# Performance work log

Measured on AMD Instinct MI355X. Metric: run time of the kernel, lower is better.

The kernel has to match this reference:

```python
import jax, jax.numpy as jnp
import numpy as np

DECAY = 0.8
BETA = 0.25
EPS = 1e-05
CODEBOOK_SIZE = 16384
CODEBOOK_DIM = 256


def setup_inputs() -> dict:
    key = jax.random.key(0)
    k1, k2 = jax.random.split(key)
    z = jax.random.normal(k1, (16, 256, 32, 32), dtype=jnp.float32)
    # EmbeddingEMA init: weight = randn(K, D) / K; embed_avg = weight.clone(); cluster_size = 0
    weight = jax.random.normal(k2, (CODEBOOK_SIZE, CODEBOOK_DIM), dtype=jnp.float32) / CODEBOOK_SIZE
    cluster_size = jnp.zeros((CODEBOOK_SIZE,), dtype=jnp.float32)
    embed_avg = weight
    return {"z": z, "weight": weight, "cluster_size": cluster_size, "embed_avg": embed_avg}


def reference(z, weight, cluster_size, embed_avg):
    K, D = weight.shape
    # b c h w -> b h w c
    zt = jnp.transpose(z, (0, 2, 3, 1))
    zf = zt.reshape(-1, D)  # [N, D]

    # squared-distance matrix [N, K]: |z|^2 + |w|^2 - 2 z.wT
    d = (jnp.sum(zf * zf, axis=1, keepdims=True)
         + jnp.sum(weight * weight, axis=1)
         - 2.0 * jnp.einsum('nd,kd->nk', zf, weight))
    token = jnp.argmin(d, axis=1)  # [N]

    z_q = weight[token].reshape(zt.shape)  # embedding lookup

    # training-mode EMA updates (scatter-add of one-hot assignments)
    counts = jax.ops.segment_sum(jnp.ones_like(token, dtype=zf.dtype), token, num_segments=K)
    embed_sum = jax.ops.segment_sum(zf, token, num_segments=K)  # one_hot.T @ zf
    cluster_new = DECAY * cluster_size + (1.0 - DECAY) * counts
    embed_avg_new = DECAY * embed_avg + (1.0 - DECAY) * embed_sum
    n = jnp.sum(cluster_new)
    smoothed = (cluster_new + EPS) / (n + K * EPS) * n
    weight_new = embed_avg_new / smoothed[:, None]

    # commitment loss (z_q detached)
    loss = BETA * jnp.mean((jax.lax.stop_gradient(z_q) - zt) ** 2)
    # straight-through estimator
    z_q_ste = zt + jax.lax.stop_gradient(z_q - zt)
    quant_error = jnp.mean(jnp.sum((z_q - zt) ** 2, axis=3))

    # codebook stats
    utilization = jnp.sum((counts > 0).astype(jnp.float32)) / K
    avg_probs = counts / jnp.sum(counts)
    perplexity = jnp.exp(-jnp.sum(avg_probs * jnp.log(avg_probs + 1e-10)))

    out = jnp.transpose(z_q_ste, (0, 3, 1, 2))  # b h w c -> b c h w
    return (out, loss, quant_error, utilization, perplexity,
            weight_new, cluster_new, embed_avg_new)
```

## Files before the change

### kernel.cpp

```cpp
#include <hip/hip_runtime.h>

#define N_TOK 16384
#define KCB   16384
#define DIM   256
#define HW    1024
#define DECAYF 0.8f
#define ONE_M_DECAY 0.2f
#define BETAF 0.25f
#define EPSF  1e-5f
#define STRIPS 8
#define KB_PER 16

typedef __attribute__((ext_vector_type(8))) short bf16x8;
typedef __attribute__((ext_vector_type(4))) float f32x4;

__device__ __forceinline__ float wave_reduce_sum(float s) {
    #pragma unroll
    for (int o = 32; o > 0; o >>= 1) s += __shfl_down(s, o);
    return s;
}

__device__ __forceinline__ unsigned short f2bf(float x) {
    union { float f; unsigned int u; } a; a.f = x;
    unsigned int r = a.u + 0x7fffu + ((a.u >> 16) & 1u);
    return (unsigned short)(r >> 16);
}

__global__ void k_transpose_z(const float* __restrict__ z, float* __restrict__ zf,
                              unsigned short* __restrict__ Ah) {
    __shared__ float t[32][33];
    int b  = blockIdx.z;
    int c0 = blockIdx.y * 32;
    int h0 = blockIdx.x * 32;
    int tid = threadIdx.x;
    int jx = tid & 31, iy = tid >> 5;
    const float* zb = z + (size_t)b * DIM * HW;
    #pragma unroll
    for (int p = 0; p < 4; ++p) {
        int ci = iy + p * 8;
        t[ci][jx] = zb[(size_t)(c0 + ci) * HW + h0 + jx];
    }
    __syncthreads();
    #pragma unroll
    for (int p = 0; p < 4; ++p) {
        int hh = iy + p * 8;
        size_t idx = (size_t)(b * HW + h0 + hh) * DIM + c0 + jx;
        float v = t[jx][hh];
        zf[idx] = v;
        Ah[idx] = f2bf(v);
    }
}

__global__ void k_prep_w(const float* __restrict__ w, unsigned short* __restrict__ Bh,
                         float* __restrict__ wnorm) {
    int wv = blockIdx.x * 4 + (threadIdx.x >> 6);
    int lane = threadIdx.x & 63;
    float4 v = ((const float4*)(w + (size_t)wv * DIM))[lane];
    ushort4 h;
    h.x = f2bf(v.x); h.y = f2bf(v.y); h.z = f2bf(v.z); h.w = f2bf(v.w);
    ((ushort4*)(Bh + (size_t)wv * DIM))[lane] = h;
    float s = v.x * v.x + v.y * v.y + v.z * v.z + v.w * v.w;
    s = wave_reduce_sum(s);
    if (lane == 0) wnorm[wv] = s;
}

__global__ void k_sum_cs(const float* __restrict__ cs, float* __restrict__ scal) {
    int i = blockIdx.x * 256 + threadIdx.x;
    int lane = threadIdx.x & 63;
    float v = cs[i];
    v = wave_reduce_sum(v);
    if (lane == 0) atomicAdd(&scal[1], v);
}

__global__ __launch_bounds__(256) void k_gemm_argmin(
    const unsigned short* __restrict__ Ah, const unsigned short* __restrict__ Bh,
    const float* __restrict__ wnorm, uint2* __restrict__ pout) {
    __shared__ unsigned short As[128 * 256];
    __shared__ unsigned short Bs[128 * 32];

    int tid  = threadIdx.x;
    int wave = tid >> 6, lane = tid & 63;
    int g16  = lane >> 4, r16 = lane & 15;
    int n0   = blockIdx.x * 128;
    int strip = blockIdx.y;

    #pragma unroll
    for (int i = 0; i < 16; ++i) {
        int s = (wave * 16 + i) * 64 + lane;
        int row = s >> 5, pos = s & 31;
        int c = pos ^ (row & 7);
        const unsigned int* ga = (const unsigned int*)(Ah + (size_t)(n0 + row) * 256 + c * 8);
        unsigned int* la = (unsigned int*)&As[(size_t)((wave * 16 + i) * 64) * 8];
        __builtin_amdgcn_global_load_lds((const __attribute__((address_space(1))) unsigned int*)ga,
                                         (__attribute__((address_space(3))) unsigned int*)la, 16, 0, 0);
    }

    unsigned int b1[16], b2[16];
    #pragma unroll
    for (int i = 0; i < 16; ++i) { b1[i] = 0xFFFFFFFFu; b2[i] = 0xFFFFFFFFu; }

    for (int kbi = 0; kbi < KB_PER; ++kbi) {
        int kb = strip * KB_PER + kbi;
        int c0 = kb * 128;

        f32x4 acc[4][4];
        #pragma unroll
        for (int mt = 0; mt < 4; ++mt)
            #pragma unroll
            for (int nt = 0; nt < 4; ++nt)
                acc[mt][nt] = (f32x4){0.f, 0.f, 0.f, 0.f};

        for (int ks = 0; ks < 8; ++ks) {
            __syncthreads();
            #pragma unroll
            for (int j = 0; j < 2; ++j) {
                int s = (wave * 2 + j) * 64 + lane;
                int m = s >> 2, pk = (s & 3) ^ (m & 3);
                const unsigned int* gb = (const unsigned int*)(Bh + (size_t)(c0 + m) * 256 + ks * 32 + pk * 8);
                unsigned int* lb = (unsigned int*)&Bs[(size_t)((wave * 2 + j) * 64) * 8];
                __builtin_amdgcn_global_load_lds((const __attribute__((address_space(1))) unsigned int*)gb,
                                                 (__attribute__((address_space(3))) unsigned int*)lb, 16, 0, 0);
            }
            __syncthreads();
            bf16x8 af[4], bfr[4];
            #pragma unroll
            for (int mt = 0; mt < 4; ++mt) {
                int row = (wave >> 1) * 64 + mt * 16 + r16;
                int pos = (ks * 4 + g16) ^ (row & 7);
                af[mt] = *(const bf16x8*)&As[(row * 32 + pos) * 8];
            }
            #pragma unroll
            for (int nt = 0; nt < 4; ++nt) {
                int row = (wave & 1) * 64 + nt * 16 + r16;
                int pk = g16 ^ (row & 3);
                bfr[nt] = *(const bf16x8*)&Bs[(row * 4 + pk) * 8];
            }
            #pragma unroll
            for (int mt = 0; mt < 4; ++mt)
                #pragma unroll
                for (int nt = 0; nt < 4; ++nt)
                    acc[mt][nt] = __builtin_amdgcn_mfma_f32_16x16x32_bf16(af[mt], bfr[nt], acc[mt][nt], 0, 0, 0);
        }

        float wnb[4];
        unsigned int orv[4];
        #pragma unroll
        for (int nt = 0; nt < 4; ++nt) {
            int code = c0 + (wave & 1) * 64 + nt * 16 + r16;
            wnb[nt] = wnorm[code] + 0.0625f;
            orv[nt] = (unsigned int)((kbi << 7) | ((wave & 1) << 6) | (nt << 4));
        }
        #pragma unroll
        for (int mt = 0; mt < 4; ++mt)
            #pragma unroll
            for (int rg = 0; rg < 4; ++rg) {
                int i = mt * 4 + rg;
                #pragma unroll
                for (int nt = 0; nt < 4; ++nt) {
                    float s = fmaf(-2.0f, acc[mt][nt][rg], wnb[nt]);
                    unsigned int u = (__float_as_uint(s) & 0xFFFFF800u) | orv[nt];
                    unsigned int t = b1[i] > u ? b1[i] : u;
                    b1[i] = b1[i] < u ? b1[i] : u;
                    b2[i] = b2[i] < t ? b2[i] : t;
                }
            }
    }

    #pragma unroll
    for (int i = 0; i < 16; ++i) {
        unsigned int v1 = b1[i] | (unsigned int)r16;
        unsigned int v2 = b2[i] | (unsigned int)r16;
        #pragma unroll
        for (int off = 1; off < 16; off <<= 1) {
            unsigned int o1 = __shfl_xor((int)v1, off);
            unsigned int o2 = __shfl_xor((int)v2, off);
            unsigned int n1 = v1 < o1 ? v1 : o1;
            unsigned int hi = v1 < o1 ? o1 : v1;
            unsigned int lo = v2 < o2 ? v2 : o2;
            v1 = n1;
            v2 = hi < lo ? hi : lo;
        }
        b1[i] = v1; b2[i] = v2;
    }

    __syncthreads();
    unsigned int* red1 = (unsigned int*)Bs;
    unsigned int* red2 = red1 + 256;
    if (r16 == 0) {
        #pragma unroll
        for (int mt = 0; mt < 4; ++mt)
            #pragma unroll
            for (int rg = 0; rg < 4; ++rg) {
                int row = (wave >> 1) * 64 + mt * 16 + g16 * 4 + rg;
                red1[(wave & 1) * 128 + row] = b1[mt * 4 + rg];
                red2[(wave & 1) * 128 + row] = b2[mt * 4 + rg];
            }
    }
    __syncthreads();
    if (tid < 128) {
        unsigned int a1 = red1[tid], a2 = red2[tid];
        unsigned int c1 = red1[128 + tid], c2 = red2[128 + tid];
        unsigned int m1 = a1 < c1 ? a1 : c1;
        unsigned int hi = a1 < c1 ? c1 : a1;
        unsigned int lo = a2 < c2 ? a2 : c2;
        pout[(size_t)strip * N_TOK + n0 + tid] = make_uint2(m1, hi < lo ? hi : lo);
    }
}

__global__ void k_select(const uint2* __restrict__ pout, const float* __restrict__ zf,
                         const float* __restrict__ w, int2* __restrict__ tokrank,
                         float* __restrict__ counts, float* __restrict__ dmin) {
    int n = blockIdx.x * 4 + (threadIdx.x >> 6);
    int lane = threadIdx.x & 63;
    unsigned int c1 = 0xFFFFFFFFu, c2 = 0xFFFFFFFFu;
    int s1 = 0, s2 = 0;
    #pragma unroll
    for (int s = 0; s < STRIPS; ++s) {
        uint2 p = pout[(size_t)s * N_TOK + n];
        if (p.x < c1)      { c2 = c1; s2 = s1; c1 = p.x; s1 = s; }
        else if (p.x < c2) { c2 = p.x; s2 = s; }
        if (p.y < c1)      { c2 = c1; s2 = s1; c1 = p.y; s1 = s; }
        else if (p.y < c2) { c2 = p.y; s2 = s; }
    }
    int code1 = (s1 << 11) | (int)(c1 & 0x7FFu);
    int code2 = (s2 << 11) | (int)(c2 & 0x7FFu);

    float4 zv = ((const float4*)(zf + (size_t)n * DIM))[lane];
    float4 w1 = ((const float4*)(w + (size_t)code1 * DIM))[lane];
    float4 w2 = ((const float4*)(w + (size_t)code2 * DIM))[lane];
    float ax = zv.x - w1.x, ay = zv.y - w1.y, az = zv.z - w1.z, aw = zv.w - w1.w;
    float bx = zv.x - w2.x, by = zv.y - w2.y, bz = zv.z - w2.z, bw = zv.w - w2.w;
    float d1 = ax * ax + ay * ay + az * az + aw * aw;
    float d2 = bx * bx + by * by + bz * bz + bw * bw;
    d1 = wave_reduce_sum(d1);
    d2 = wave_reduce_sum(d2);
    if (lane == 0) {
        bool take2 = (d2 < d1) || (d2 == d1 && code2 < code1);
        int tok = take2 ? code2 : code1;
        dmin[n] = take2 ? d2 : d1;
        float old = atomicAdd(&counts[tok], 1.0f);
        tokrank[n] = make_int2(tok, (int)old);
    }
}

__global__ void k_scan(const float* __restrict__ counts, int* __restrict__ offsets) {
    int tid = threadIdx.x;
    int lane = tid & 63, wv = tid >> 6;
    int base = tid * 64;
    int sum = 0;
    for (int i = 0; i < 64; ++i) sum += (int)counts[base + i];
    int x = sum;
    #pragma unroll
    for (int o = 1; o < 64; o <<= 1) {
        int y = __shfl_up(x, o);
        if (lane >= o) x += y;
    }
    __shared__ int wt[4];
    if (lane == 63) wt[wv] = x;
    __syncthreads();
    int wbase = 0;
    for (int i = 0; i < wv; ++i) wbase += wt[i];
    int run = wbase + x - sum;
    for (int i = 0; i < 64; ++i) {
        offsets[base + i] = run;
        run += (int)counts[base + i];
    }
}

__global__ void k_scatter(const int2* __restrict__ tokrank, const int* __restrict__ offsets,
                          int* __restrict__ perm) {
    int n = blockIdx.x * 256 + threadIdx.x;
    int2 tr = tokrank[n];
    perm[offsets[tr.x] + tr.y] = n;
}

__global__ void k_embed(const int* __restrict__ offsets, const float* __restrict__ counts,
                        const int* __restrict__ perm, const float* __restrict__ zf,
                        const float* __restrict__ ea, const float* __restrict__ cs,
                        const float* __restrict__ scal, float* __restrict__ o_embed,
                        float* __restrict__ o_cluster, float* __restrict__ o_wnew) {
    int k = blockIdx.x * 4 + (threadIdx.x >> 6);
    int lane = threadIdx.x & 63;
    int off = offsets[k];
    int c = (int)counts[k];
    float4 acc = make_float4(0.f, 0.f, 0.f, 0.f);
    for (int i = 0; i < c; ++i) {
        int n = perm[off + i];
        float4 zv = ((const float4*)(zf + (size_t)n * DIM))[lane];
        acc.x += zv.x; acc.y += zv.y; acc.z += zv.z; acc.w += zv.w;
    }
    float4 eav = ((const float4*)(ea + (size_t)k * DIM))[lane];
    float4 em = make_float4(DECAYF * eav.x + ONE_M_DECAY * acc.x,
                            DECAYF * eav.y + ONE_M_DECAY * acc.y,
                            DECAYF * eav.z + ONE_M_DECAY * acc.z,
                            DECAYF * eav.w + ONE_M_DECAY * acc.w);
    ((float4*)(o_embed + (size_t)k * DIM))[lane] = em;
    float cn = DECAYF * cs[k] + ONE_M_DECAY * (float)c;
    float ntot = DECAYF * scal[1] + ONE_M_DECAY * (float)N_TOK;
    float sm = (cn + EPSF) / (ntot + (float)KCB * EPSF) * ntot;
    float inv = 1.0f / sm;
    ((float4*)(o_wnew + (size_t)k * DIM))[lane] =
        make_float4(em.x * inv, em.y * inv, em.z * inv, em.w * inv);
    if (lane == 0) o_cluster[k] = cn;
}

__global__ void k_write_out(const int2* __restrict__ tokrank, const float* __restrict__ w,
                            float* __restrict__ out) {
    __shared__ float t[32][33];
    __shared__ int tok[32];
    int b = blockIdx.z, c0 = blockIdx.y * 32, h0 = blockIdx.x * 32;
    int tid = threadIdx.x, jx = tid & 31, iy = tid >> 5;
    if (tid < 32) tok[tid] = tokrank[b * HW + h0 + tid].x;
    __syncthreads();
    #pragma unroll
    for (int p = 0; p < 4; ++p) {
        int hh = iy + p * 8;
        t[hh][jx] = w[(size_t)tok[hh] * DIM + c0 + jx];
    }
    __syncthreads();
    #pragma unroll
    for (int p = 0; p < 4; ++p) {
        int cc = iy + p * 8;
        out[(size_t)b * DIM * HW + (size_t)(c0 + cc) * HW + h0 + jx] = t[jx][cc];
    }
}

__global__ void k_stats(const float* __restrict__ counts, const float* __restrict__ dmin,
                        float* __restrict__ scal) {
    int k = blockIdx.x * 256 + threadIdx.x;
    int lane = threadIdx.x & 63;
    float cnt = counts[k];
    float used = cnt > 0.f ? 1.f : 0.f;
    float p = cnt * (1.0f / 16384.0f);
    float pl = p * logf(p + 1e-10f);
    float dv = dmin[k];
    used = wave_reduce_sum(used);
    pl   = wave_reduce_sum(pl);
    dv   = wave_reduce_sum(dv);
    if (lane == 0) {
        atomicAdd(&scal[2], used);
        atomicAdd(&scal[3], pl);
        atomicAdd(&scal[0], dv);
    }
}

__global__ void k_scalars(const float* __restrict__ scal, float* __restrict__ o_scal) {
    if (threadIdx.x == 0) {
        float sumsq = scal[0], used = scal[2], plogp = scal[3];
        o_scal[0] = BETAF * sumsq / (float)(N_TOK * DIM);
        o_scal[1] = sumsq / (float)N_TOK;
        o_scal[2] = used * (1.0f / (float)KCB);
        o_scal[3] = expf(-plogp);
    }
}

extern "C" void kernel_launch(void* const* d_in, const int* in_sizes, int n_in,
                              void* d_out, int out_size, void* d_ws, size_t ws_size,
                              hipStream_t stream) {
    const float* z  = (const float*)d_in[0];
    const float* w  = (const float*)d_in[1];
    const float* cs = (const float*)d_in[2];
    const float* ea = (const float*)d_in[3];
    float* out = (float*)d_out;

    char* w8 = (char*)d_ws;
    unsigned short* Ah = (unsigned short*)(w8 + 0);
    unsigned short* Bh = (unsigned short*)(w8 + 8388608);
    float* wnorm   = (float*)(w8 + 16777216);
    int2*  tokrank = (int2*)(w8 + 16842752);
    float* counts  = (float*)(w8 + 16973824);
    int*   offsets = (int*)(w8 + 17039360);
    int*   perm    = (int*)(w8 + 17104896);
    float* scal    = (float*)(w8 + 17170432);
    float* dmin    = (float*)(w8 + 17170496);

    float* zf = out;
    uint2* pout = (uint2*)(out + 4194308);
    float* o_scal    = out + 4194304;
    float* o_wnew    = out + 4194308;
    float* o_cluster = out + 8388612;
    float* o_embed   = out + 8404996;

    hipMemsetAsync(counts, 0, 17170432 + 64 - 16973824, stream);
    k_transpose_z<<<dim3(32, 8, 16), 256, 0, stream>>>(z, zf, Ah);
    k_prep_w<<<4096, 256, 0, stream>>>(w, Bh, wnorm);
    k_sum_cs<<<64, 256, 0, stream>>>(cs, scal);
    k_gemm_argmin<<<dim3(128, STRIPS), 256, 0, stream>>>(Ah, Bh, wnorm, pout);
    k_select<<<4096, 256, 0, stream>>>(pout, zf, w, tokrank, counts, dmin);
    k_scan<<<1, 256, 0, stream>>>(counts, offsets);
    k_scatter<<<64, 256, 0, stream>>>(tokrank, offsets, perm);
    k_embed<<<4096, 256, 0, stream>>>(offsets, counts, perm, zf, ea, cs, scal,
                                      o_embed, o_cluster, o_wnew);
    k_write_out<<<dim3(32, 8, 16), 256, 0, stream>>>(tokrank, w, out);
    k_stats<<<64, 256, 0, stream>>>(counts, dmin, scal);
    k_scalars<<<1, 64, 0, stream>>>(scal, o_scal);
}
```

Baseline: 331.2 us.

## Double-buffer codebook tile loads in GEMM-argmin with async prefetch

Splits the shared codebook (B) tile into two buffers and prefetches the next k-slice via global_load_lds while the current one feeds MFMAs, using explicit vmcnt waits and raw barriers instead of __syncthreads. It also raises wave priority around the MFMA block. This is meant to hide global-load latency that previously serialized each k-step, at the cost of extra LDS and the correctness risk of hand-managed waitcnt counts, since the A-tile loads issued before the loop also count toward vmcnt.

```diff
diff --git a/kernel.cpp b/kernel.cpp
--- a/kernel.cpp
+++ b/kernel.cpp
@@ -76,7 +76,7 @@
     const unsigned short* __restrict__ Ah, const unsigned short* __restrict__ Bh,
     const float* __restrict__ wnorm, uint2* __restrict__ pout) {
     __shared__ unsigned short As[128 * 256];
-    __shared__ unsigned short Bs[128 * 32];
+    __shared__ unsigned short Bs[2][128 * 32];
 
     int tid  = threadIdx.x;
     int wave = tid >> 6, lane = tid & 63;
@@ -95,13 +95,28 @@
                                          (__attribute__((address_space(3))) unsigned int*)la, 16, 0, 0);
     }
 
+    auto stageB = [&](int t, int buf) {
+        int kb = t >> 3, ks = t & 7;
+        int c0 = (strip * KB_PER + kb) * 128;
+        #pragma unroll
+        for (int j = 0; j < 2; ++j) {
+            int s = (wave * 2 + j) * 64 + lane;
+            int m = s >> 2, pk = (s & 3) ^ (m & 3);
+            const unsigned int* gb = (const unsigned int*)(Bh + (size_t)(c0 + m) * 256 + ks * 32 + pk * 8);
+            unsigned int* lb = (unsigned int*)&Bs[buf][(size_t)((wave * 2 + j) * 64) * 8];
+            __builtin_amdgcn_global_load_lds((const __attribute__((address_space(1))) unsigned int*)gb,
+                                             (__attribute__((address_space(3))) unsigned int*)lb, 16, 0, 0);
+        }
+    };
+
+    stageB(0, 0);
+
     unsigned int b1[16], b2[16];
     #pragma unroll
     for (int i = 0; i < 16; ++i) { b1[i] = 0xFFFFFFFFu; b2[i] = 0xFFFFFFFFu; }
 
     for (int kbi = 0; kbi < KB_PER; ++kbi) {
-        int kb = strip * KB_PER + kbi;
-        int c0 = kb * 128;
+        int c0 = (strip * KB_PER + kbi) * 128;
 
         f32x4 acc[4][4];
         #pragma unroll
@@ -111,17 +126,16 @@
                 acc[mt][nt] = (f32x4){0.f, 0.f, 0.f, 0.f};
 
         for (int ks = 0; ks < 8; ++ks) {
-            __syncthreads();
-            #pragma unroll
-            for (int j = 0; j < 2; ++j) {
-                int s = (wave * 2 + j) * 64 + lane;
-                int m = s >> 2, pk = (s & 3) ^ (m & 3);
-                const unsigned int* gb = (const unsigned int*)(Bh + (size_t)(c0 + m) * 256 + ks * 32 + pk * 8);
-                unsigned int* lb = (unsigned int*)&Bs[(size_t)((wave * 2 + j) * 64) * 8];
-                __builtin_amdgcn_global_load_lds((const __attribute__((address_space(1))) unsigned int*)gb,
-                                                 (__attribute__((address_space(3))) unsigned int*)lb, 16, 0, 0);
+            int t = kbi * 8 + ks;
+            if (t < KB_PER * 8 - 1) {
+                stageB(t + 1, (t + 1) & 1);
+                asm volatile("s_waitcnt vmcnt(2)" ::: "memory");
+            } else {
+                asm volatile("s_waitcnt vmcnt(0)" ::: "memory");
             }
-            __syncthreads();
+            __builtin_amdgcn_s_barrier();
+            asm volatile("" ::: "memory");
+
             bf16x8 af[4], bfr[4];
             #pragma unroll
             for (int mt = 0; mt < 4; ++mt) {
@@ -133,13 +147,17 @@
             for (int nt = 0; nt < 4; ++nt) {
                 int row = (wave & 1) * 64 + nt * 16 + r16;
                 int pk = g16 ^ (row & 3);
-                bfr[nt] = *(const bf16x8*)&Bs[(row * 4 + pk) * 8];
+                bfr[nt] = *(const bf16x8*)&Bs[t & 1][(row * 4 + pk) * 8];
             }
+            __builtin_amdgcn_s_setprio(1);
             #pragma unroll
             for (int mt = 0; mt < 4; ++mt)
                 #pragma unroll
                 for (int nt = 0; nt < 4; ++nt)
                     acc[mt][nt] = __builtin_amdgcn_mfma_f32_16x16x32_bf16(af[mt], bfr[nt], acc[mt][nt], 0, 0, 0);
+            __builtin_amdgcn_s_setprio(0);
+            asm volatile("" ::: "memory");
+            __builtin_amdgcn_s_barrier();
         }
 
         float wnb[4];
@@ -159,9 +177,9 @@
                 for (int nt = 0; nt < 4; ++nt) {
                     float s = fmaf(-2.0f, acc[mt][nt][rg], wnb[nt]);
                     unsigned int u = (__float_as_uint(s) & 0xFFFFF800u) | orv[nt];
-                    unsigned int t = b1[i] > u ? b1[i] : u;
+                    unsigned int t2 = b1[i] > u ? b1[i] : u;
                     b1[i] = b1[i] < u ? b1[i] : u;
-                    b2[i] = b2[i] < t ? b2[i] : t;
+                    b2[i] = b2[i] < t2 ? b2[i] : t2;
                 }
             }
     }
```

Measured after the change: 331.8 us. About the same (+0.2%).

## Load codebook fragments directly to registers with 3-deep prefetch, drop B LDS tile

Applied to the files above, without the earlier changes.

The GEMM-argmin kernel no longer stages codebook tiles through shared memory with two barriers per k-step. Each wave loads its B fragments straight from global memory into registers, keeping a ring of four register buffers that are prefetched three steps ahead. MFMA issue priority is raised around the inner product, and launch bounds ask for two blocks per CU. This removes per-step barriers and LDS traffic, but adds register pressure and uncoalesced 16-byte global loads, and each B fragment is now fetched redundantly by the waves that share it.

```diff
diff --git a/kernel.cpp b/kernel.cpp
--- a/kernel.cpp
+++ b/kernel.cpp
@@ -72,11 +72,10 @@
     if (lane == 0) atomicAdd(&scal[1], v);
 }
 
-__global__ __launch_bounds__(256) void k_gemm_argmin(
+__global__ __launch_bounds__(256, 2) void k_gemm_argmin(
     const unsigned short* __restrict__ Ah, const unsigned short* __restrict__ Bh,
     const float* __restrict__ wnorm, uint2* __restrict__ pout) {
     __shared__ unsigned short As[128 * 256];
-    __shared__ unsigned short Bs[128 * 32];
 
     int tid  = threadIdx.x;
     int wave = tid >> 6, lane = tid & 63;
@@ -95,13 +94,31 @@
                                          (__attribute__((address_space(3))) unsigned int*)la, 16, 0, 0);
     }
 
+    int boff[4];
+    #pragma unroll
+    for (int nt = 0; nt < 4; ++nt) {
+        int row = (wave & 1) * 64 + nt * 16 + r16;
+        boff[nt] = row * 256 + g16 * 8;
+    }
+    const unsigned short* Bbase = Bh + (size_t)strip * KB_PER * 128 * 256;
+
+    bf16x8 pf[4][4];
+    #pragma unroll
+    for (int t = 0; t < 3; ++t) {
+        const unsigned short* bp = Bbase + t * 32;
+        #pragma unroll
+        for (int nt = 0; nt < 4; ++nt)
+            pf[t][nt] = *(const bf16x8*)(bp + boff[nt]);
+    }
+
+    __syncthreads();
+
     unsigned int b1[16], b2[16];
     #pragma unroll
     for (int i = 0; i < 16; ++i) { b1[i] = 0xFFFFFFFFu; b2[i] = 0xFFFFFFFFu; }
 
     for (int kbi = 0; kbi < KB_PER; ++kbi) {
-        int kb = strip * KB_PER + kbi;
-        int c0 = kb * 128;
+        int c0 = (strip * KB_PER + kbi) * 128;
 
         f32x4 acc[4][4];
         #pragma unroll
@@ -110,36 +127,30 @@
             for (int nt = 0; nt < 4; ++nt)
                 acc[mt][nt] = (f32x4){0.f, 0.f, 0.f, 0.f};
 
+        #pragma unroll
         for (int ks = 0; ks < 8; ++ks) {
-            __syncthreads();
-            #pragma unroll
-            for (int j = 0; j < 2; ++j) {
-                int s = (wave * 2 + j) * 64 + lane;
-                int m = s >> 2, pk = (s & 3) ^ (m & 3);
-                const unsigned int* gb = (const unsigned int*)(Bh + (size_t)(c0 + m) * 256 + ks * 32 + pk * 8);
-                unsigned int* lb = (unsigned int*)&Bs[(size_t)((wave * 2 + j) * 64) * 8];
-                __builtin_amdgcn_global_load_lds((const __attribute__((address_space(1))) unsigned int*)gb,
-                                                 (__attribute__((address_space(3))) unsigned int*)lb, 16, 0, 0);
-            }
-            __syncthreads();
-            bf16x8 af[4], bfr[4];
+            int kb3 = kbi + (ks >= 5 ? 1 : 0);
+            if (kb3 > KB_PER - 1) kb3 = KB_PER - 1;
+            int ks3 = (ks + 3) & 7;
+            const unsigned short* bp = Bbase + (size_t)kb3 * 32768 + ks3 * 32;
+            #pragma unroll
+            for (int nt = 0; nt < 4; ++nt)
+                pf[(ks + 3) & 3][nt] = *(const bf16x8*)(bp + boff[nt]);
+
+            bf16x8 af[4];
             #pragma unroll
             for (int mt = 0; mt < 4; ++mt) {
                 int row = (wave >> 1) * 64 + mt * 16 + r16;
                 int pos = (ks * 4 + g16) ^ (row & 7);
                 af[mt] = *(const bf16x8*)&As[(row * 32 + pos) * 8];
             }
-            #pragma unroll
-            for (int nt = 0; nt < 4; ++nt) {
-                int row = (wave & 1) * 64 + nt * 16 + r16;
-                int pk = g16 ^ (row & 3);
-                bfr[nt] = *(const bf16x8*)&Bs[(row * 4 + pk) * 8];
-            }
+            __builtin_amdgcn_s_setprio(1);
             #pragma unroll
             for (int mt = 0; mt < 4; ++mt)
                 #pragma unroll
                 for (int nt = 0; nt < 4; ++nt)
-                    acc[mt][nt] = __builtin_amdgcn_mfma_f32_16x16x32_bf16(af[mt], bfr[nt], acc[mt][nt], 0, 0, 0);
+                    acc[mt][nt] = __builtin_amdgcn_mfma_f32_16x16x32_bf16(af[mt], pf[ks & 3][nt], acc[mt][nt], 0, 0, 0);
+            __builtin_amdgcn_s_setprio(0);
         }
 
         float wnb[4];
@@ -159,9 +170,9 @@
                 for (int nt = 0; nt < 4; ++nt) {
                     float s = fmaf(-2.0f, acc[mt][nt][rg], wnb[nt]);
                     unsigned int u = (__float_as_uint(s) & 0xFFFFF800u) | orv[nt];
-                    unsigned int t = b1[i] > u ? b1[i] : u;
+                    unsigned int t2 = b1[i] > u ? b1[i] : u;
                     b1[i] = b1[i] < u ? b1[i] : u;
-                    b2[i] = b2[i] < t ? b2[i] : t;
+                    b2[i] = b2[i] < t2 ? b2[i] : t2;
                 }
             }
     }
@@ -184,7 +195,7 @@
     }
 
     __syncthreads();
-    unsigned int* red1 = (unsigned int*)Bs;
+    unsigned int* red1 = (unsigned int*)As;
     unsigned int* red2 = red1 + 256;
     if (r16 == 0) {
         #pragma unroll
```

After: 639.1 us. 93.0% more time.
